# Kernel optimization log

Measured on AMD Instinct MI355X. Metric: run time of the kernel, lower is better.

The kernel has to match this reference:

```python
import jax, jax.numpy as jnp
import numpy as np

N = 50000      # nodes
E = 800000     # edges (before self-loops)
IN_DIM = 128
HID = 64
OUT = 32
HEADS = 8
BN_EPS = 1e-5
NEG_SLOPE = 0.2  # PyG GATConv default


def setup_inputs() -> dict:
    key = jax.random.key(0)
    ks = jax.random.split(key, 24)
    g = lambda k, shape, fan_in: (jax.random.normal(k, shape, jnp.float32) / np.sqrt(fan_in))
    return {
        "x": jax.random.normal(ks[0], (N, IN_DIM), jnp.float32),
        "edge_index": jax.random.randint(ks[1], (2, E), 0, N, dtype=jnp.int64),
        # GCN1
        "gcn1_w": g(ks[2], (IN_DIM, HID), IN_DIM),
        "gcn1_b": jnp.zeros((HID,), jnp.float32),
        # BN1 (eval mode running stats)
        "bn1_gamma": jnp.ones((HID,), jnp.float32),
        "bn1_beta": jnp.zeros((HID,), jnp.float32),
        "bn1_mean": 0.1 * jax.random.normal(ks[3], (HID,), jnp.float32),
        "bn1_var": 0.5 + jax.random.uniform(ks[4], (HID,), jnp.float32),
        # GAT1: heads=8, per-head out=HID, concat=False -> mean over heads
        "gat1_w": g(ks[5], (HID, HEADS * HID), HID),
        "gat1_asrc": g(ks[6], (HEADS, HID), HID),
        "gat1_adst": g(ks[7], (HEADS, HID), HID),
        "gat1_b": jnp.zeros((HID,), jnp.float32),
        # GCN2
        "gcn2_w": g(ks[8], (HID, HID), HID),
        "gcn2_b": jnp.zeros((HID,), jnp.float32),
        # BN2
        "bn2_gamma": jnp.ones((HID,), jnp.float32),
        "bn2_beta": jnp.zeros((HID,), jnp.float32),
        "bn2_mean": 0.1 * jax.random.normal(ks[9], (HID,), jnp.float32),
        "bn2_var": 0.5 + jax.random.uniform(ks[10], (HID,), jnp.float32),
        # GAT2: heads=8, per-head out=OUT, concat=False
        "gat2_w": g(ks[11], (HID, HEADS * OUT), HID),
        "gat2_asrc": g(ks[12], (HEADS, OUT), OUT),
        "gat2_adst": g(ks[13], (HEADS, OUT), OUT),
        "gat2_b": jnp.zeros((OUT,), jnp.float32),
    }


def _gcn(x, src, dst, w, b, n):
    # PyG GCNConv: x @ W, symmetric norm with self-loops (src/dst already include them)
    h = x @ w
    deg = jax.ops.segment_sum(jnp.ones(src.shape[0], x.dtype), dst, num_segments=n)
    dinv = jnp.where(deg > 0, jax.lax.rsqrt(jnp.maximum(deg, 1.0)), 0.0)
    coef = dinv[src] * dinv[dst]                     # [E']
    out = jax.ops.segment_sum(coef[:, None] * h[src], dst, num_segments=n)
    return out + b


def _gat(x, src, dst, w, a_src, a_dst, b, n, heads, ch):
    # PyG GATConv (concat=False): mean over heads, softmax over incoming edges per dst
    h = (x @ w).reshape(n, heads, ch)                # [N,H,C]
    es = jnp.einsum('nhc,hc->nh', h, a_src)          # alpha_src per node
    ed = jnp.einsum('nhc,hc->nh', h, a_dst)
    e = jax.nn.leaky_relu(es[src] + ed[dst], NEG_SLOPE)  # [E',H]
    m = jax.ops.segment_max(e, dst, num_segments=n)
    m = jnp.where(jnp.isfinite(m), m, 0.0)
    ex = jnp.exp(e - m[dst])
    denom = jax.ops.segment_sum(ex, dst, num_segments=n)
    alpha = ex / (denom[dst] + 1e-16)                # [E',H]
    out = jnp.zeros((n, ch), x.dtype)
    for hd in range(heads):  # fixed small head loop keeps peak edge memory at [E',C]
        msg = alpha[:, hd, None] * h[src, hd]        # [E',C]
        out = out + jax.ops.segment_sum(msg, dst, num_segments=n)
    return out / heads + b


def _bn_eval(x, gamma, beta, mean, var):
    return (x - mean) * jax.lax.rsqrt(var + BN_EPS) * gamma + beta


def reference(x, edge_index,
              gcn1_w, gcn1_b, bn1_gamma, bn1_beta, bn1_mean, bn1_var,
              gat1_w, gat1_asrc, gat1_adst, gat1_b,
              gcn2_w, gcn2_b, bn2_gamma, bn2_beta, bn2_mean, bn2_var,
              gat2_w, gat2_asrc, gat2_adst, gat2_b):
    n = x.shape[0]
    loops = jnp.arange(n, dtype=edge_index.dtype)
    src = jnp.concatenate([edge_index[0], loops])    # self-loops (PyG default)
    dst = jnp.concatenate([edge_index[1], loops])

    h = _gcn(x, src, dst, gcn1_w, gcn1_b, n)
    h = jax.nn.relu(_bn_eval(h, bn1_gamma, bn1_beta, bn1_mean, bn1_var))
    h = jax.nn.relu(_gat(h, src, dst, gat1_w, gat1_asrc, gat1_adst, gat1_b, n, HEADS, HID))
    h = _gcn(h, src, dst, gcn2_w, gcn2_b, n)
    h = jax.nn.relu(_bn_eval(h, bn2_gamma, bn2_beta, bn2_mean, bn2_var))
    h = _gat(h, src, dst, gat2_w, gat2_asrc, gat2_adst, gat2_b, n, HEADS, OUT)
    return jax.nn.log_softmax(h, axis=1)
```

## Files before the change

### kernel.cpp

```cpp
#include <hip/hip_runtime.h>
#include <hip/hip_bf16.h>

#define NN 50000
#define NE 800000
#define IND 128
#define NH 8
#define EBLK 256
#define EPB 3125
#define NBUK 391
#define NBUKP 392
#define GH (NBUKP * EBLK)
#define PREPB 308

typedef __hip_bfloat16 bf16;
typedef __attribute__((ext_vector_type(8))) short short8;
typedef __attribute__((ext_vector_type(8))) __bf16 bf16x8;
typedef __attribute__((ext_vector_type(4))) float floatx4;
typedef __attribute__((ext_vector_type(2))) float floatx2;

static __device__ __forceinline__ short f2bf_bits(float f) {
    unsigned u = __float_as_uint(f);
    u = (u + 0x7fffu + ((u >> 16) & 1u)) >> 16;
    return (short)u;
}
// ... 19 lines not shown
static __device__ __forceinline__ void scan_buckets(const int* __restrict__ bsum,
        int* sp, int* gb, int tid) {
    int v0 = (2 * tid < NBUKP) ? bsum[2 * tid] : 0;
    int v1 = (2 * tid + 1 < NBUKP) ? bsum[2 * tid + 1] : 0;
    int c = v0 + v1;
    sp[tid] = c; __syncthreads();
    int val = c;
#pragma unroll
    for (int off = 1; off < 256; off <<= 1) {
        int t = (tid >= off) ? sp[tid - off] : 0;
        __syncthreads();
        val += t; sp[tid] = val;
        __syncthreads();
    }
    int pex = val - c;
    gb[2 * tid] = pex;
    gb[2 * tid + 1] = pex + v0;
    __syncthreads();
}

__global__ __launch_bounds__(256) void bin_count_prep_kernel(const int* __restrict__ edst,
        int* __restrict__ ghist,
        const float* __restrict__ gcn1_w, const float* __restrict__ gcn2_w,
        const float* __restrict__ gat1_w, const float* __restrict__ gat2_w,
        const float* __restrict__ as1, const float* __restrict__ ad1,
        const float* __restrict__ as2, const float* __restrict__ ad2,
        bf16* __restrict__ wT1, bf16* __restrict__ wT2,
        bf16* __restrict__ wgT1, bf16* __restrict__ wgT2,
        float* __restrict__ was1, float* __restrict__ wad1,
        float* __restrict__ was2, float* __restrict__ wad2) {
    __shared__ int hsh[NBUKP];
    const int tid = threadIdx.x;
    if (blockIdx.x < EBLK) {
        const int blk = blockIdx.x;
        for (int b = tid; b < NBUKP; b += 256) hsh[b] = 0;
        __syncthreads();
        const int e0 = blk * EPB;
        for (int e = e0 + tid; e < e0 + EPB; e += 256)
            atomicAdd(&hsh[edst[e] >> 7], 1);
        __syncthreads();
        for (int b = tid; b < NBUKP; b += 256)
            ghist[b * EBLK + blk] = hsh[b];
    } else {
        int idx = (blockIdx.x - EBLK) * 256 + tid;
        if (idx < 8192) {
            int m = idx >> 7, k = idx & 127;
            ((short*)wT1)[idx] = f2bf_bits(gcn1_w[(long)k * 64 + m]);
        } else if (idx < 12288) {
            int i = idx - 8192;
            int m = i >> 6, k = i & 63;
            ((short*)wT2)[i] = f2bf_bits(gcn2_w[(long)k * 64 + m]);
        } else if (idx < 45056) {
            int i = idx - 12288;
            int m = i >> 9, k = i & 511;
            int h = k >> 6, c = k & 63;
            ((short*)wgT1)[i] = f2bf_bits(gat1_w[(long)c * 512 + h * 64 + m]);
        } else if (idx < 77824) {
            int i = idx - 45056;
            int m = i >> 9, k = i & 511;
            int h = k >> 6, c = k & 63;
            ((short*)wgT2)[i] = (m < 32) ? f2bf_bits(gat2_w[(long)c * 256 + h * 32 + m]) : (short)0;
        } else if (idx < 78336) {
            int i = idx - 77824;
            int h = i >> 6, c = i & 63;
            const float* wrow = gat1_w + (long)c * 512 + h * 64;
            float s = 0.f, d = 0.f;
            for (int cc = 0; cc < 64; ++cc) {
                float w = wrow[cc];
                s += w * as1[h * 64 + cc];
                d += w * ad1[h * 64 + cc];
            }
            was1[i] = s; wad1[i] = d;
        } else if (idx < 78848) {
            int i = idx - 78336;
            int h = i >> 6, c = i & 63;
            const float* wrow = gat2_w + (long)c * 256 + h * 32;
            float s = 0.f, d = 0.f;
            for (int cc = 0; cc < 32; ++cc) {
                float w = wrow[cc];
                s += w * as2[h * 32 + cc];
                d += w * ad2[h * 32 + cc];
            }
            was2[i] = s; wad2[i] = d;
        }
    }
}

__global__ __launch_bounds__(256) void scang1_kernel(const int* __restrict__ src,
        int* __restrict__ pre, int* __restrict__ bsum, int n) {
    __shared__ int sh[256];
    const int tid = threadIdx.x;
    const int idx = blockIdx.x * 256 + tid;
    int c = (idx < n) ? src[idx] : 0;
    sh[tid] = c; __syncthreads();
    int val = c;
#pragma unroll
    for (int off = 1; off < 256; off <<= 1) {
        int t = (tid >= off) ? sh[tid - off] : 0;
        __syncthreads();
        val += t; sh[tid] = val;
        __syncthreads();
    }
    if (idx < n) pre[idx] = val - c;
    if (tid == 255) bsum[blockIdx.x] = val;
}

__global__ __launch_bounds__(256) void bin_scatter_kernel(const int* __restrict__ esrc,
        const int* __restrict__ edst, const int* __restrict__ gpre,
        const int* __restrict__ bsum, unsigned* __restrict__ ebuf) {
    __shared__ int cur[NBUKP];
    __shared__ int sp[256], gb[512];
    const int tid = threadIdx.x, blk = blockIdx.x;
    scan_buckets(bsum, sp, gb, tid);
    for (int b = tid; b < NBUKP; b += 256)
        cur[b] = gpre[b * EBLK + blk] + gb[b];
    __syncthreads();
    const int e0 = blk * EPB;
    for (int e = e0 + tid; e < e0 + EPB; e += 256) {
        int d = edst[e], s = esrc[e];
        int pos = atomicAdd(&cur[d >> 7], 1);
        ebuf[pos] = ((unsigned)(d & 127) << 16) | (unsigned)s;
    }
}

__global__ __launch_bounds__(256) void bucket_finalize_kernel(const unsigned* __restrict__ ebuf,
        const int* __restrict__ gpre, const int* __restrict__ bsum,
        int* __restrict__ rowptr, float* __restrict__ dinv, int* __restrict__ csrc) {
    __shared__ int lh[128], lcur[128], sc[256];
    __shared__ int sp[256], gb[512];
    const int bu = blockIdx.x, tid = threadIdx.x;
    scan_buckets(bsum, sp, gb, tid);
    const int seg_beg = gpre[bu * EBLK] + gb[bu];
    const int seg_end = gpre[(bu + 1) * EBLK] + gb[bu + 1];
    if (tid < 128) lh[tid] = 0;
    __syncthreads();
    for (int i = seg_beg + tid; i < seg_end; i += 256)
        atomicAdd(&lh[ebuf[i] >> 16], 1);
    __syncthreads();
    int c = (tid < 128) ? lh[tid] : 0;
    sc[tid] = c; __syncthreads();
    int val = c;
#pragma unroll
    for (int off = 1; off < 256; off <<= 1) {
        int t = (tid >= off) ? sc[tid - off] : 0;
        __syncthreads();
        val += t; sc[tid] = val;
        __syncthreads();
    }
    int excl = val - c;
    if (tid < 128) {
        lcur[tid] = excl;
        int node = bu * 128 + tid;
        if (node < NN) {
            rowptr[node] = seg_beg + excl;
            dinv[node] = rsqrtf((float)c + 1.f);
        }
    }
    if (bu == 0 && tid == 0) rowptr[NN] = NE;
    __syncthreads();
    for (int i = seg_beg + tid; i < seg_end; i += 256) {
        unsigned u = ebuf[i];
        int pos = atomicAdd(&lcur[u >> 16], 1);
        csrc[seg_beg + pos] = (int)(u & 0xffffu);
    }
}

template<int K, int EPI, bool AF32>
__global__ __launch_bounds__(256) void mm2_kernel(const void* __restrict__ A,
        const bf16* __restrict__ wT, void* __restrict__ C,
        const float* __restrict__ bias, const float* __restrict__ rowscale,
        int nrows, int M) {
    const int row0 = blockIdx.x * 64;
    const int tid = threadIdx.x;
    const int lane = tid & 63, wave = tid >> 6;
    const int lr = lane & 15, q = lane >> 4;
    const int row = row0 + wave * 16 + lr;
    const bool rok = row < nrows;
    constexpr int NC = 4;
    floatx4 acc[NC] = {};
#pragma unroll 4
    for (int k0 = 0; k0 < K; k0 += 32) {
        short8 av = {0, 0, 0, 0, 0, 0, 0, 0};
        if (rok) {
            if (AF32) {
                const float* apf = (const float*)A + (long)row * K + q * 8 + k0;
                floatx4 va = *(const floatx4*)apf;
                floatx4 vb = *(const floatx4*)(apf + 4);
#pragma unroll
                for (int j = 0; j < 4; ++j) { av[j] = f2bf_bits(va[j]); av[4 + j] = f2bf_bits(vb[j]); }
            } else {
                av = *(const short8*)((const short*)A + (long)row * K + q * 8 + k0);
            }
        }
        bf16x8 a = __builtin_bit_cast(bf16x8, av);
#pragma unroll
        for (int c = 0; c < NC; ++c) {
            bf16x8 b = __builtin_bit_cast(bf16x8,
                *(const short8*)((const short*)wT + (long)(c * 16 + lr) * K + k0 + q * 8));
            acc[c] = __builtin_amdgcn_mfma_f32_16x16x32_bf16(a, b, acc[c], 0, 0, 0);
        }
    }
#pragma unroll
    for (int c = 0; c < NC; ++c)
#pragma unroll
        for (int r = 0; r < 4; ++r) {
            int orow = row0 + wave * 16 + q * 4 + r;
            int col = c * 16 + lr;
            if (orow < nrows && col < M) {
                long o = (long)orow * M + col;
                float v = acc[c][r];
                if (EPI == 0) ((float*)C)[o] = v;
                else if (EPI == 2) {
                    v = v * 0.125f + bias[col];
                    ((bf16*)C)[o] = __float2bfloat16(fmaxf(v, 0.f));
                } else {
                    ((bf16*)C)[o] = __float2bfloat16(rowscale[orow] * v);
                }
            }
        }
}

__global__ __launch_bounds__(256) void gcn_fused_kernel(const int* __restrict__ rowptr,
        const int* __restrict__ csrc, const float* __restrict__ dinv,
        const bf16* __restrict__ hin, const float* __restrict__ b,
        const float* __restrict__ gamma, const float* __restrict__ beta,
        const float* __restrict__ mean, const float* __restrict__ var,
        bf16* __restrict__ actout) {
    const int node = blockIdx.x * 4 + (threadIdx.x >> 6);
    if (node >= NN) return;
    const int lane = threadIdx.x & 63;
    const int eslot = lane >> 5, cp = lane & 31;
    const unsigned cpo = 4u * (unsigned)cp;
    const int beg = __builtin_amdgcn_readfirstlane(rowptr[node]);
    const int end = __builtin_amdgcn_readfirstlane(rowptr[node + 1]);
    const float di = dinv[node];
    const int* csp = csrc + beg;
    floatx2 acc2 = {0.f, 0.f};
    const int dn = end - beg;
    const int kup = (dn + 15) & ~15;
    for (int k0 = 0; k0 < kup; k0 += 16) {
        int s_[8]; float w_[8];
#pragma unroll
        for (int u = 0; u < 8; ++u) {
            int k = k0 + 2 * u + eslot;
            int ok = k < dn;
            s_[u] = csp[ok ? k : 0];
            w_[u] = ok ? 1.f : 0.f;
        }
        unsigned av_[8];
#pragma unroll
        for (int u = 0; u < 8; ++u)
            av_[u] = *(const unsigned*)((const char*)hin + ((unsigned)s_[u] * 128u + cpo));
#pragma unroll
        for (int u = 0; u < 8; ++u) {
            floatx2 a2 = up2(av_[u]);
            acc2 += a2 * w_[u];
        }
    }
    acc2.x += __shfl_xor(acc2.x, 32);
    acc2.y += __shfl_xor(acc2.y, 32);
    {
        unsigned sv = *(const unsigned*)((const char*)hin + ((unsigned)node * 128u + cpo));
        acc2 += up2(sv);
    }
    int c0 = 2 * cp, c1 = c0 + 1;
    float x0 = acc2.x * di + b[c0];
    float x1 = acc2.y * di + b[c1];
    x0 = (x0 - mean[c0]) * rsqrtf(var[c0] + 1e-5f) * gamma[c0] + beta[c0];
    x1 = (x1 - mean[c1]) * rsqrtf(var[c1] + 1e-5f) * gamma[c1] + beta[c1];
    if (eslot == 0)
        *(unsigned*)((unsigned short*)actout + (long)node * 64 + c0) =
            pk2(fmaxf(x0, 0.f), fmaxf(x1, 0.f));
}

__global__ __launch_bounds__(256) void scores_kernel(const bf16* __restrict__ actb,
        const float* __restrict__ was, const float* __restrict__ wad,
        float* __restrict__ es, float* __restrict__ ed, int n) {
    const int node = blockIdx.x * 4 + (threadIdx.x >> 6);
    if (node >= n) return;
    const int lane = threadIdx.x & 63;
    const int h = lane >> 3, cg = lane & 7;
    short8 a8 = *(const short8*)((const short*)actb + (long)node * 64 + cg * 8);
    const float* wsp = was + h * 64 + cg * 8;
    const float* wdp = wad + h * 64 + cg * 8;
    floatx4 ws0 = *(const floatx4*)wsp, ws1 = *(const floatx4*)(wsp + 4);
    floatx4 wd0 = *(const floatx4*)wdp, wd1 = *(const floatx4*)(wdp + 4);
    float s = 0.f, d = 0.f;
#pragma unroll
    for (int j = 0; j < 4; ++j) {
        float v0 = bf2f(__builtin_bit_cast(bf16, a8[j]));
        float v1 = bf2f(__builtin_bit_cast(bf16, a8[4 + j]));
        s += v0 * ws0[j] + v1 * ws1[j];
        d += v0 * wd0[j] + v1 * wd1[j];
    }
#pragma unroll
    for (int off = 1; off < 8; off <<= 1) {
        s += __shfl_xor(s, off);
        d += __shfl_xor(d, off);
    }
    if (cg == 0) { es[node * NH + h] = s; ed[node * NH + h] = d; }
}

template<int NCT, int EPI>
__global__ __launch_bounds__(256) void gat_fused_kernel(const int* __restrict__ rowptr,
        const int* __restrict__ csrc, const float* __restrict__ es, const float* __restrict__ ed,
        const bf16* __restrict__ actb, const bf16* __restrict__ wgT,
        const float* __restrict__ bias, void* __restrict__ outp) {
    __shared__ __align__(16) float salpha[4][512];
    __shared__ int ssrcs[4][64];
    __shared__ __align__(16) float sself[4][8];
    __shared__ __align__(16) unsigned short aggt[16][520];
    __shared__ float redbuf[2][2][16];
    const int wv = threadIdx.x >> 6;
    const int lane = threadIdx.x & 63;
    const int h = lane & 7, slot = lane >> 3;
    const int hq = lane >> 5, cp = lane & 31;
    const unsigned cpo = 4u * (unsigned)cp;

#pragma unroll 1
    for (int nn = 0; nn < 4; ++nn) {
        const int row = wv * 4 + nn;
        const int node = blockIdx.x * 16 + row;
        const int beg = __builtin_amdgcn_readfirstlane(rowptr[node]);
        const int end = __builtin_amdgcn_readfirstlane(rowptr[node + 1]);
        const int deg = end - beg;
        const int* csp = csrc + beg;
        const float edr = *(const float*)((const char*)ed + ((unsigned)node * 32u + (unsigned)h * 4u));
        float selfe = *(const float*)((const char*)es + ((unsigned)node * 32u + (unsigned)h * 4u)) + edr;
        selfe = selfe > 0.f ? selfe : 0.2f * selfe;

        if (deg <= 64) {
            const int nb = (deg + 7) >> 3;
            const int dm1 = (deg > 0) ? deg - 1 : 0;
            float ex_r[8]; int s_r[8];
            float den = 0.f;
#pragma unroll
            for (int b = 0; b < 8; ++b) { ex_r[b] = 0.f; s_r[b] = 0; }
            if (deg > 0) {
#pragma unroll
                for (int b = 0; b < 8; ++b)
                    if (b < nb) {
                        int k = b * 8 + slot;
                        s_r[b] = csp[k < deg ? k : dm1];
                    }
#pragma unroll
                for (int b = 0; b < 8; ++b)
                    if (b < nb) {
                        float e = *(const float*)((const char*)es +
                                  ((unsigned)s_r[b] * 32u + (unsigned)h * 4u)) + edr;
                        e = e > 0.f ? e : 0.2f * e;
                        float ex = __expf(e - selfe);
                        ex_r[b] = (b * 8 + slot < deg) ? ex : 0.f;
                        den += ex_r[b];
                    }
            }
            den += __shfl_xor(den, 8);
            den += __shfl_xor(den, 16);
            den += __shfl_xor(den, 32);
            const float invden = 1.f / (den + 1.f);
#pragma unroll
            for (int b = 0; b < 8; ++b)
                if (b < nb) salpha[wv][b * 64 + lane] = ex_r[b] * invden;
            if (h == 0) {
#pragma unroll
                for (int b = 0; b < 8; ++b)
                    if (b < nb) ssrcs[wv][b * 8 + slot] = s_r[b];
            }
            if (slot == 0) sself[wv][h] = invden;

            floatx2 acc2[4] = {};
            const int ng = nb;
            if (ng > 0) {
                int sA0, sA1, sA2, sA3, sA4, sA5, sA6, sA7;
                int sB0, sB1, sB2, sB3, sB4, sB5, sB6, sB7;
                unsigned rA0, rA1, rA2, rA3, rA4, rA5, rA6, rA7;
                unsigned rB0, rB1, rB2, rB3, rB4, rB5, rB6, rB7;
#define LOAD_BANK(S, R, G) do { \
    const int* sp_ = &ssrcs[wv][(G) * 8]; \
    S##0 = __builtin_amdgcn_readfirstlane(sp_[0]); \
    S##1 = __builtin_amdgcn_readfirstlane(sp_[1]); \
    S##2 = __builtin_amdgcn_readfirstlane(sp_[2]); \
    S##3 = __builtin_amdgcn_readfirstlane(sp_[3]); \
    S##4 = __builtin_amdgcn_readfirstlane(sp_[4]); \
    S##5 = __builtin_amdgcn_readfirstlane(sp_[5]); \
    S##6 = __builtin_amdgcn_readfirstlane(sp_[6]); \
    S##7 = __builtin_amdgcn_readfirstlane(sp_[7]); \
    R##0 = *(const unsigned*)((const char*)actb + ((unsigned)S##0 * 128u + cpo)); \
    R##1 = *(const unsigned*)((const char*)actb + ((unsigned)S##1 * 128u + cpo)); \
    R##2 = *(const unsigned*)((const char*)actb + ((unsigned)S##2 * 128u + cpo)); \
    R##3 = *(const unsigned*)((const char*)actb + ((unsigned)S##3 * 128u + cpo)); \
    R##4 = *(const unsigned*)((const char*)actb + ((unsigned)S##4 * 128u + cpo)); \
    R##5 = *(const unsigned*)((const char*)actb + ((unsigned)S##5 * 128u + cpo)); \
    R##6 = *(const unsigned*)((const char*)actb + ((unsigned)S##6 * 128u + cpo)); \
    R##7 = *(const unsigned*)((const char*)actb + ((unsigned)S##7 * 128u + cpo)); \
} while (0)
#define FMA_BANK(R, G) do { \
    const float* ab_ = &salpha[wv][(G) * 64 + hq * 4]; \
    unsigned rr_[8] = {R##0, R##1, R##2, R##3, R##4, R##5, R##6, R##7}; \
    _Pragma("unroll") \
    for (int j_ = 0; j_ < 8; ++j_) { \
        floatx4 al_ = *(const floatx4*)(ab_ + j_ * 8); \
        floatx2 al01_ = __builtin_shufflevector(al_, al_, 0, 1); \
        floatx2 al23_ = __builtin_shufflevector(al_, al_, 2, 3); \
        floatx2 a2_ = up2(rr_[j_]); \
        pk_fma_lo(acc2[0], a2_, al01_); pk_fma_hi(acc2[1], a2_, al01_); \
        pk_fma_lo(acc2[2], a2_, al23_); pk_fma_hi(acc2[3], a2_, al23_); \
    } \
} while (0)
                LOAD_BANK(sA, rA, 0);
                int g = 0;
                while (true) {
                    if (g + 1 < ng) LOAD_BANK(sB, rB, g + 1);
                    __builtin_amdgcn_sched_barrier(0);
                    FMA_BANK(rA, g);
                    ++g; if (g >= ng) break;
                    if (g + 1 < ng) LOAD_BANK(sA, rA, g + 1);
                    __builtin_amdgcn_sched_barrier(0);
                    FMA_BANK(rB, g);
                    ++g; if (g >= ng) break;
                }
#undef LOAD_BANK
#undef FMA_BANK
            }
            {
                unsigned sv = *(const unsigned*)((const char*)actb + ((unsigned)node * 128u + cpo));
                floatx2 a2 = up2(sv);
                floatx4 sa = *(const floatx4*)&sself[wv][hq * 4];
                floatx2 sa01 = __builtin_shufflevector(sa, sa, 0, 1);
                floatx2 sa23 = __builtin_shufflevector(sa, sa, 2, 3);
                pk_fma_lo(acc2[0], a2, sa01); pk_fma_hi(acc2[1], a2, sa01);
                pk_fma_lo(acc2[2], a2, sa23); pk_fma_hi(acc2[3], a2, sa23);
            }
#pragma unroll
            for (int j = 0; j < 4; ++j)
                *(unsigned*)&aggt[row][(hq * 4 + j) * 64 + 2 * cp] = pk2(acc2[j].x, acc2[j].y);
        } else {
            float acc[NH] = {0.f, 0.f, 0.f, 0.f, 0.f, 0.f, 0.f, 0.f};
            float den = 0.f;
            for (int base = beg; base < end; base += 8) {
                int ei = base + slot;
                if (ei < end) {
                    int s = csrc[ei];
                    float e = es[s * NH + h] + edr;
                    e = e > 0.f ? e : 0.2f * e;
                    den += __expf(e - selfe);
                }
            }
            den += __shfl_xor(den, 8);
            den += __shfl_xor(den, 16);
            den += __shfl_xor(den, 32);
            const float invden = 1.f / (den + 1.f);
            for (int base = beg; base < end; base += 8) {
                int ei = base + slot;
                float al = 0.f; int sl = 0;
                if (ei < end) {
                    sl = csrc[ei];
                    float e = es[sl * NH + h] + edr;
                    e = e > 0.f ? e : 0.2f * e;
                    al = __expf(e - selfe) * invden;
                }
                salpha[wv][lane] = al;
                if (h == 0) ssrcs[wv][slot] = sl;
                int ecnt = end - base; if (ecnt > 8) ecnt = 8;
                for (int j = 0; j < ecnt; ++j) {
                    int s = ssrcs[wv][j];
                    float a = bf2f(actb[(long)s * 64 + lane]);
                    floatx4 al0 = *(const floatx4*)&salpha[wv][j * 8];
                    floatx4 al1 = *(const floatx4*)&salpha[wv][j * 8 + 4];
                    acc[0] += al0[0] * a; acc[1] += al0[1] * a;
                    acc[2] += al0[2] * a; acc[3] += al0[3] * a;
                    acc[4] += al1[0] * a; acc[5] += al1[1] * a;
                    acc[6] += al1[2] * a; acc[7] += al1[3] * a;
                }
            }
            {
                if (slot == 0) sself[wv][h] = invden;
                float a = bf2f(actb[(long)node * 64 + lane]);
                floatx4 s0 = *(const floatx4*)&sself[wv][0];
                floatx4 s1 = *(const floatx4*)&sself[wv][4];
                acc[0] += s0[0] * a; acc[1] += s0[1] * a;
                acc[2] += s0[2] * a; acc[3] += s0[3] * a;
                acc[4] += s1[0] * a; acc[5] += s1[1] * a;
                acc[6] += s1[2] * a; acc[7] += s1[3] * a;
            }
#pragma unroll
            for (int hh = 0; hh < NH; ++hh)
                aggt[row][hh * 64 + lane] = (unsigned short)f2bf_bits(acc[hh]);
        }
    }

    __syncthreads();

    const int lr = lane & 15, q = lane >> 4;
    const bool act = wv < NCT;
    floatx4 acc = {};
    if (act) {
#pragma unroll 4
        for (int k0 = 0; k0 < 512; k0 += 32) {
            bf16x8 a = __builtin_bit_cast(bf16x8,
                *(const short8*)&aggt[lr][k0 + q * 8]);
            bf16x8 b = __builtin_bit_cast(bf16x8,
                *(const short8*)((const short*)wgT + (long)(wv * 16 + lr) * 512 + k0 + q * 8));
            acc = __builtin_amdgcn_mfma_f32_16x16x32_bf16(a, b, acc, 0, 0, 0);
        }
    }

    if (EPI == 2) {
        if (act) {
#pragma unroll
            for (int r = 0; r < 4; ++r) {
                int node = blockIdx.x * 16 + q * 4 + r;
                int col = wv * 16 + lr;
                float v = acc[r] * 0.125f + bias[col];
                ((bf16*)outp)[(long)node * 64 + col] = __float2bfloat16(fmaxf(v, 0.f));
            }
        }
    } else {
        float v[4], m[4];
#pragma unroll
        for (int r = 0; r < 4; ++r) {
            v[r] = acc[r] * 0.125f + (act ? bias[wv * 16 + lr] : 0.f);
            m[r] = v[r];
        }
#pragma unroll
        for (int off = 1; off < 16; off <<= 1)
#pragma unroll
            for (int r = 0; r < 4; ++r) m[r] = fmaxf(m[r], __shfl_xor(m[r], off));
        if (act && lr == 0) {
#pragma unroll
            for (int r = 0; r < 4; ++r) redbuf[0][wv][q * 4 + r] = m[r];
        }
        __syncthreads();
        float s[4];
#pragma unroll
        for (int r = 0; r < 4; ++r) {
            float mm_ = fmaxf(redbuf[0][0][q * 4 + r], redbuf[0][1][q * 4 + r]);
            m[r] = mm_;
            s[r] = act ? __expf(v[r] - mm_) : 0.f;
        }
#pragma unroll
        for (int off = 1; off < 16; off <<= 1)
#pragma unroll
            for (int r = 0; r < 4; ++r) s[r] += __shfl_xor(s[r], off);
        if (act && lr == 0) {
#pragma unroll
            for (int r = 0; r < 4; ++r) redbuf[1][wv][q * 4 + r] = s[r];
        }
        __syncthreads();
        if (act) {
#pragma unroll
            for (int r = 0; r < 4; ++r) {
                int row = q * 4 + r;
                int node = blockIdx.x * 16 + row;
                float ls = m[r] + logf(redbuf[1][0][row] + redbuf[1][1][row]);
                ((float*)outp)[(long)node * 32 + wv * 16 + lr] = v[r] - ls;
            }
        }
    }
}

extern "C" void kernel_launch(void* const* d_in, const int* in_sizes, int n_in,
                              void* d_out, int out_size, void* d_ws, size_t ws_size,
                              hipStream_t stream) {
    const float* x        = (const float*)d_in[0];
    const int*   eidx     = (const int*)d_in[1];
    const float* gcn1_w   = (const float*)d_in[2];
    const float* gcn1_b   = (const float*)d_in[3];
    const float* bn1_g    = (const float*)d_in[4];
    const float* bn1_b    = (const float*)d_in[5];
    const float* bn1_m    = (const float*)d_in[6];
    const float* bn1_v    = (const float*)d_in[7];
    const float* gat1_w   = (const float*)d_in[8];
    const float* gat1_as  = (const float*)d_in[9];
    const float* gat1_ad  = (const float*)d_in[10];
    const float* gat1_b   = (const float*)d_in[11];
    const float* gcn2_w   = (const float*)d_in[12];
    const float* gcn2_b   = (const float*)d_in[13];
    const float* bn2_g    = (const float*)d_in[14];
    const float* bn2_b    = (const float*)d_in[15];
    const float* bn2_m    = (const float*)d_in[16];
    const float* bn2_v    = (const float*)d_in[17];
    const float* gat2_w   = (const float*)d_in[18];
    const float* gat2_as  = (const float*)d_in[19];
    const float* gat2_ad  = (const float*)d_in[20];
    const float* gat2_b   = (const float*)d_in[21];
    float* out = (float*)d_out;

    const int* esrc = eidx;
    const int* edst = eidx + NE;

    float* ws = (float*)d_ws;
    int*      ghist  = (int*)ws;
    int*      gpre   = ghist + GH;
    int*      gbsum  = gpre + GH;
    unsigned* ebuf   = (unsigned*)(gbsum + 512);
    int*      rowptr = (int*)(ebuf + NE);
    int*      csrc   = rowptr + 50048;
    float*    dinv   = (float*)(csrc + NE);
    float*    es     = dinv + 50048;
    float*    ed     = es + 400000;
    float*    was1   = ed + 400000;
    float*    wad1   = was1 + 512;
    float*    was2   = wad1 + 512;
    float*    wad2   = was2 + 512;
    bf16*     wT1    = (bf16*)(wad2 + 512);
    bf16*     wT2    = wT1 + 64 * 128;
    bf16*     wgT1   = wT2 + 64 * 64;
    bf16*     wgT2   = wgT1 + 64 * 512;
    bf16*     actb   = wgT2 + 64 * 512;
    bf16*     mmbf   = actb + (size_t)NN * 64;
    bf16*     gact   = mmbf + (size_t)NN * 64;

    auto cdiv = [](long a, long b) { return (int)((a + b - 1) / b); };
    const int GB = cdiv(NN, 64);
    const int NB = cdiv(NN, 4);
    const int FB = NN / 16;

    bin_count_prep_kernel<<<EBLK + PREPB, 256, 0, stream>>>(edst, ghist,
        gcn1_w, gcn2_w, gat1_w, gat2_w, gat1_as, gat1_ad, gat2_as, gat2_ad,
        wT1, wT2, wgT1, wgT2, was1, wad1, was2, wad2);
    scang1_kernel<<<GH / 256, 256, 0, stream>>>(ghist, gpre, gbsum, GH);
    bin_scatter_kernel<<<EBLK, 256, 0, stream>>>(esrc, edst, gpre, gbsum, ebuf);
    bucket_finalize_kernel<<<NBUK, 256, 0, stream>>>(ebuf, gpre, gbsum, rowptr, dinv, csrc);

    mm2_kernel<IND, 3, true><<<GB, 256, 0, stream>>>(x, wT1, mmbf, nullptr, dinv, NN, 64);
    gcn_fused_kernel<<<NB, 256, 0, stream>>>(rowptr, csrc, dinv, mmbf,
        gcn1_b, bn1_g, bn1_b, bn1_m, bn1_v, actb);

    scores_kernel<<<NB, 256, 0, stream>>>(actb, was1, wad1, es, ed, NN);
    gat_fused_kernel<4, 2><<<FB, 256, 0, stream>>>(rowptr, csrc, es, ed, actb, wgT1, gat1_b, gact);

    mm2_kernel<64, 3, false><<<GB, 256, 0, stream>>>(gact, wT2, mmbf, nullptr, dinv, NN, 64);
    gcn_fused_kernel<<<NB, 256, 0, stream>>>(rowptr, csrc, dinv, mmbf,
        gcn2_b, bn2_g, bn2_b, bn2_m, bn2_v, actb);

    scores_kernel<<<NB, 256, 0, stream>>>(actb, was2, wad2, es, ed, NN);
    gat_fused_kernel<2, 4><<<FB, 256, 0, stream>>>(rowptr, csrc, es, ed, actb, wgT2, gat2_b, out);
}
```

Baseline: 347.6 us.

## Process four nodes per GAT block instead of sixteen to raise block count

The fused GAT kernel now assigns one node per wavefront (4 nodes per block) instead of looping each wave over 4 nodes (16 per block), quadrupling the grid size. Unused rows of the 16-row aggregation tile are zeroed so the MFMA projection epilogue still runs on a full tile, but only the first 4 rows are written out. The aim is more parallelism and latency hiding for the irregular gather. In exchange, most of the projection matmul work is wasted on zero rows, and each block pays extra fixed costs (zero-fill, reloading weights).

```diff
diff --git a/kernel.cpp b/kernel.cpp
--- a/kernel.cpp
+++ b/kernel.cpp
@@ -353,71 +353,71 @@
     __shared__ int ssrcs[4][64];
     __shared__ __align__(16) float sself[4][8];
     __shared__ __align__(16) unsigned short aggt[16][520];
-    __shared__ float redbuf[2][2][16];
+    __shared__ float redbuf[2][2][4];
     const int wv = threadIdx.x >> 6;
     const int lane = threadIdx.x & 63;
     const int h = lane & 7, slot = lane >> 3;
     const int hq = lane >> 5, cp = lane & 31;
     const unsigned cpo = 4u * (unsigned)cp;
 
-#pragma unroll 1
-    for (int nn = 0; nn < 4; ++nn) {
-        const int row = wv * 4 + nn;
-        const int node = blockIdx.x * 16 + row;
-        const int beg = __builtin_amdgcn_readfirstlane(rowptr[node]);
-        const int end = __builtin_amdgcn_readfirstlane(rowptr[node + 1]);
-        const int deg = end - beg;
-        const int* csp = csrc + beg;
-        const float edr = *(const float*)((const char*)ed + ((unsigned)node * 32u + (unsigned)h * 4u));
-        float selfe = *(const float*)((const char*)es + ((unsigned)node * 32u + (unsigned)h * 4u)) + edr;
-        selfe = selfe > 0.f ? selfe : 0.2f * selfe;
-
-        if (deg <= 64) {
-            const int nb = (deg + 7) >> 3;
-            const int dm1 = (deg > 0) ? deg - 1 : 0;
-            float ex_r[8]; int s_r[8];
-            float den = 0.f;
-#pragma unroll
-            for (int b = 0; b < 8; ++b) { ex_r[b] = 0.f; s_r[b] = 0; }
-            if (deg > 0) {
-#pragma unroll
-                for (int b = 0; b < 8; ++b)
-                    if (b < nb) {
-                        int k = b * 8 + slot;
-                        s_r[b] = csp[k < deg ? k : dm1];
-                    }
-#pragma unroll
-                for (int b = 0; b < 8; ++b)
-                    if (b < nb) {
-                        float e = *(const float*)((const char*)es +
-                                  ((unsigned)s_r[b] * 32u + (unsigned)h * 4u)) + edr;
-                        e = e > 0.f ? e : 0.2f * e;
-                        float ex = __expf(e - selfe);
-                        ex_r[b] = (b * 8 + slot < deg) ? ex : 0.f;
-                        den += ex_r[b];
-                    }
-            }
-            den += __shfl_xor(den, 8);
-            den += __shfl_xor(den, 16);
-            den += __shfl_xor(den, 32);
-            const float invden = 1.f / (den + 1.f);
+    for (int i = threadIdx.x; i < 12 * 260; i += 256)
+        ((unsigned*)&aggt[4][0])[i] = 0u;
+
+    const int node = blockIdx.x * 4 + wv;
+    const int beg = __builtin_amdgcn_readfirstlane(rowptr[node]);
+    const int end = __builtin_amdgcn_readfirstlane(rowptr[node + 1]);
+    const int deg = end - beg;
+    const int* csp = csrc + beg;
+    const float edr = *(const float*)((const char*)ed + ((unsigned)node * 32u + (unsigned)h * 4u));
+    float selfe = *(const float*)((const char*)es + ((unsigned)node * 32u + (unsigned)h * 4u)) + edr;
+    selfe = selfe > 0.f ? selfe : 0.2f * selfe;
+
+    if (deg <= 64) {
+        const int nb = (deg + 7) >> 3;
+        const int dm1 = (deg > 0) ? deg - 1 : 0;
+        float ex_r[8]; int s_r[8];
+        float den = 0.f;
+#pragma unroll
+        for (int b = 0; b < 8; ++b) { ex_r[b] = 0.f; s_r[b] = 0; }
+        if (deg > 0) {
 #pragma unroll
             for (int b = 0; b < 8; ++b)
-                if (b < nb) salpha[wv][b * 64 + lane] = ex_r[b] * invden;
-            if (h == 0) {
-#pragma unroll
-                for (int b = 0; b < 8; ++b)
-                    if (b < nb) ssrcs[wv][b * 8 + slot] = s_r[b];
-            }
-            if (slot == 0) sself[wv][h] = invden;
-
-            floatx2 acc2[4] = {};
-            const int ng = nb;
-            if (ng > 0) {
-                int sA0, sA1, sA2, sA3, sA4, sA5, sA6, sA7;
-                int sB0, sB1, sB2, sB3, sB4, sB5, sB6, sB7;
-                unsigned rA0, rA1, rA2, rA3, rA4, rA5, rA6, rA7;
-                unsigned rB0, rB1, rB2, rB3, rB4, rB5, rB6, rB7;
+                if (b < nb) {
+                    int k = b * 8 + slot;
+                    s_r[b] = csp[k < deg ? k : dm1];
+                }
+#pragma unroll
+            for (int b = 0; b < 8; ++b)
+                if (b < nb) {
+                    float e = *(const float*)((const char*)es +
+                              ((unsigned)s_r[b] * 32u + (unsigned)h * 4u)) + edr;
+                    e = e > 0.f ? e : 0.2f * e;
+                    float ex = __expf(e - selfe);
+                    ex_r[b] = (b * 8 + slot < deg) ? ex : 0.f;
+                    den += ex_r[b];
+                }
+        }
+        den += __shfl_xor(den, 8);
+        den += __shfl_xor(den, 16);
+        den += __shfl_xor(den, 32);
+        const float invden = 1.f / (den + 1.f);
+#pragma unroll
+        for (int b = 0; b < 8; ++b)
+            if (b < nb) salpha[wv][b * 64 + lane] = ex_r[b] * invden;
+        if (h == 0) {
+#pragma unroll
+            for (int b = 0; b < 8; ++b)
+                if (b < nb) ssrcs[wv][b * 8 + slot] = s_r[b];
+        }
+        if (slot == 0) sself[wv][h] = invden;
+
+        floatx2 acc2[4] = {};
+        const int ng = nb;
+        if (ng > 0) {
+            int sA0, sA1, sA2, sA3, sA4, sA5, sA6, sA7;
+            int sB0, sB1, sB2, sB3, sB4, sB5, sB6, sB7;
+            unsigned rA0, rA1, rA2, rA3, rA4, rA5, rA6, rA7;
+            unsigned rB0, rB1, rB2, rB3, rB4, rB5, rB6, rB7;
 #define LOAD_BANK(S, R, G) do { \
     const int* sp_ = &ssrcs[wv][(G) * 8]; \
     S##0 = __builtin_amdgcn_readfirstlane(sp_[0]); \
@@ -450,86 +450,85 @@
         pk_fma_lo(acc2[2], a2_, al23_); pk_fma_hi(acc2[3], a2_, al23_); \
     } \
 } while (0)
-                LOAD_BANK(sA, rA, 0);
-                int g = 0;
-                while (true) {
-                    if (g + 1 < ng) LOAD_BANK(sB, rB, g + 1);
-                    __builtin_amdgcn_sched_barrier(0);
-                    FMA_BANK(rA, g);
-                    ++g; if (g >= ng) break;
-                    if (g + 1 < ng) LOAD_BANK(sA, rA, g + 1);
-                    __builtin_amdgcn_sched_barrier(0);
-                    FMA_BANK(rB, g);
-                    ++g; if (g >= ng) break;
-                }
+            LOAD_BANK(sA, rA, 0);
+            int g = 0;
+            while (true) {
+                if (g + 1 < ng) LOAD_BANK(sB, rB, g + 1);
+                __builtin_amdgcn_sched_barrier(0);
+                FMA_BANK(rA, g);
+                ++g; if (g >= ng) break;
+                if (g + 1 < ng) LOAD_BANK(sA, rA, g + 1);
+                __builtin_amdgcn_sched_barrier(0);
+                FMA_BANK(rB, g);
+                ++g; if (g >= ng) break;
+            }
 #undef LOAD_BANK
 #undef FMA_BANK
-            }
-            {
-                unsigned sv = *(const unsigned*)((const char*)actb + ((unsigned)node * 128u + cpo));
-                floatx2 a2 = up2(sv);
-                floatx4 sa = *(const floatx4*)&sself[wv][hq * 4];
-                floatx2 sa01 = __builtin_shufflevector(sa, sa, 0, 1);
-                floatx2 sa23 = __builtin_shufflevector(sa, sa, 2, 3);
-                pk_fma_lo(acc2[0], a2, sa01); pk_fma_hi(acc2[1], a2, sa01);
-                pk_fma_lo(acc2[2], a2, sa23); pk_fma_hi(acc2[3], a2, sa23);
-            }
-#pragma unroll
-            for (int j = 0; j < 4; ++j)
-                *(unsigned*)&aggt[row][(hq * 4 + j) * 64 + 2 * cp] = pk2(acc2[j].x, acc2[j].y);
-        } else {
-            float acc[NH] = {0.f, 0.f, 0.f, 0.f, 0.f, 0.f, 0.f, 0.f};
-            float den = 0.f;
-            for (int base = beg; base < end; base += 8) {
-                int ei = base + slot;
-                if (ei < end) {
-                    int s = csrc[ei];
-                    float e = es[s * NH + h] + edr;
-                    e = e > 0.f ? e : 0.2f * e;
-                    den += __expf(e - selfe);
-                }
-            }
-            den += __shfl_xor(den, 8);
-            den += __shfl_xor(den, 16);
-            den += __shfl_xor(den, 32);
-            const float invden = 1.f / (den + 1.f);
-            for (int base = beg; base < end; base += 8) {
-                int ei = base + slot;
-                float al = 0.f; int sl = 0;
-                if (ei < end) {
-                    sl = csrc[ei];
-                    float e = es[sl * NH + h] + edr;
-                    e = e > 0.f ? e : 0.2f * e;
-                    al = __expf(e - selfe) * invden;
-                }
-                salpha[wv][lane] = al;
-                if (h == 0) ssrcs[wv][slot] = sl;
-                int ecnt = end - base; if (ecnt > 8) ecnt = 8;
-                for (int j = 0; j < ecnt; ++j) {
-                    int s = ssrcs[wv][j];
-                    float a = bf2f(actb[(long)s * 64 + lane]);
-                    floatx4 al0 = *(const floatx4*)&salpha[wv][j * 8];
-                    floatx4 al1 = *(const floatx4*)&salpha[wv][j * 8 + 4];
-                    acc[0] += al0[0] * a; acc[1] += al0[1] * a;
-                    acc[2] += al0[2] * a; acc[3] += al0[3] * a;
-                    acc[4] += al1[0] * a; acc[5] += al1[1] * a;
-                    acc[6] += al1[2] * a; acc[7] += al1[3] * a;
-                }
-            }
-            {
-                if (slot == 0) sself[wv][h] = invden;
-                float a = bf2f(actb[(long)node * 64 + lane]);
-                floatx4 s0 = *(const floatx4*)&sself[wv][0];
-                floatx4 s1 = *(const floatx4*)&sself[wv][4];
-                acc[0] += s0[0] * a; acc[1] += s0[1] * a;
-                acc[2] += s0[2] * a; acc[3] += s0[3] * a;
-                acc[4] += s1[0] * a; acc[5] += s1[1] * a;
-                acc[6] += s1[2] * a; acc[7] += s1[3] * a;
-            }
-#pragma unroll
-            for (int hh = 0; hh < NH; ++hh)
-                aggt[row][hh * 64 + lane] = (unsigned short)f2bf_bits(acc[hh]);
-        }
+        }
+        {
+            unsigned sv = *(const unsigned*)((const char*)actb + ((unsigned)node * 128u + cpo));
+            floatx2 a2 = up2(sv);
+            floatx4 sa = *(const floatx4*)&sself[wv][hq * 4];
+            floatx2 sa01 = __builtin_shufflevector(sa, sa, 0, 1);
+            floatx2 sa23 = __builtin_shufflevector(sa, sa, 2, 3);
+            pk_fma_lo(acc2[0], a2, sa01); pk_fma_hi(acc2[1], a2, sa01);
+            pk_fma_lo(acc2[2], a2, sa23); pk_fma_hi(acc2[3], a2, sa23);
+        }
+#pragma unroll
+        for (int j = 0; j < 4; ++j)
+            *(unsigned*)&aggt[wv][(hq * 4 + j) * 64 + 2 * cp] = pk2(acc2[j].x, acc2[j].y);
+    } else {
+        float acc[NH] = {0.f, 0.f, 0.f, 0.f, 0.f, 0.f, 0.f, 0.f};
+        float den = 0.f;
+        for (int base = beg; base < end; base += 8) {
+            int ei = base + slot;
+            if (ei < end) {
+                int s = csrc[ei];
+                float e = es[s * NH + h] + edr;
+                e = e > 0.f ? e : 0.2f * e;
+                den += __expf(e - selfe);
+            }
+        }
+        den += __shfl_xor(den, 8);
+        den += __shfl_xor(den, 16);
+        den += __shfl_xor(den, 32);
+        const float invden = 1.f / (den + 1.f);
+        for (int base = beg; base < end; base += 8) {
+            int ei = base + slot;
+            float al = 0.f; int sl = 0;
+            if (ei < end) {
+                sl = csrc[ei];
+                float e = es[sl * NH + h] + edr;
+                e = e > 0.f ? e : 0.2f * e;
+                al = __expf(e - selfe) * invden;
+            }
+            salpha[wv][lane] = al;
+            if (h == 0) ssrcs[wv][slot] = sl;
+            int ecnt = end - base; if (ecnt > 8) ecnt = 8;
+            for (int j = 0; j < ecnt; ++j) {
+                int s = ssrcs[wv][j];
+                float a = bf2f(actb[(long)s * 64 + lane]);
+                floatx4 al0 = *(const floatx4*)&salpha[wv][j * 8];
+                floatx4 al1 = *(const floatx4*)&salpha[wv][j * 8 + 4];
+                acc[0] += al0[0] * a; acc[1] += al0[1] * a;
+                acc[2] += al0[2] * a; acc[3] += al0[3] * a;
+                acc[4] += al1[0] * a; acc[5] += al1[1] * a;
+                acc[6] += al1[2] * a; acc[7] += al1[3] * a;
+            }
+        }
+        {
+            if (slot == 0) sself[wv][h] = invden;
+            float a = bf2f(actb[(long)node * 64 + lane]);
+            floatx4 s0 = *(const floatx4*)&sself[wv][0];
+            floatx4 s1 = *(const floatx4*)&sself[wv][4];
+            acc[0] += s0[0] * a; acc[1] += s0[1] * a;
+            acc[2] += s0[2] * a; acc[3] += s0[3] * a;
+            acc[4] += s1[0] * a; acc[5] += s1[1] * a;
+            acc[6] += s1[2] * a; acc[7] += s1[3] * a;
+        }
+#pragma unroll
+        for (int hh = 0; hh < NH; ++hh)
+            aggt[wv][hh * 64 + lane] = (unsigned short)f2bf_bits(acc[hh]);
     }
 
     __syncthreads();
@@ -549,13 +548,13 @@
     }
 
     if (EPI == 2) {
-        if (act) {
+        if (act && q == 0) {
 #pragma unroll
             for (int r = 0; r < 4; ++r) {
-                int node = blockIdx.x * 16 + q * 4 + r;
+                int onode = blockIdx.x * 4 + r;
                 int col = wv * 16 + lr;
                 float v = acc[r] * 0.125f + bias[col];
-                ((bf16*)outp)[(long)node * 64 + col] = __float2bfloat16(fmaxf(v, 0.f));
+                ((bf16*)outp)[(long)onode * 64 + col] = __float2bfloat16(fmaxf(v, 0.f));
             }
         }
     } else {
@@ -569,15 +568,15 @@
         for (int off = 1; off < 16; off <<= 1)
 #pragma unroll
             for (int r = 0; r < 4; ++r) m[r] = fmaxf(m[r], __shfl_xor(m[r], off));
-        if (act && lr == 0) {
-#pragma unroll
-            for (int r = 0; r < 4; ++r) redbuf[0][wv][q * 4 + r] = m[r];
+        if (act && q == 0 && lr == 0) {
+#pragma unroll
+            for (int r = 0; r < 4; ++r) redbuf[0][wv][r] = m[r];
         }
         __syncthreads();
         float s[4];
 #pragma unroll
         for (int r = 0; r < 4; ++r) {
-            float mm_ = fmaxf(redbuf[0][0][q * 4 + r], redbuf[0][1][q * 4 + r]);
+            float mm_ = fmaxf(redbuf[0][0][r], redbuf[0][1][r]);
             m[r] = mm_;
             s[r] = act ? __expf(v[r] - mm_) : 0.f;
         }
@@ -585,18 +584,17 @@
         for (int off = 1; off < 16; off <<= 1)
 #pragma unroll
             for (int r = 0; r < 4; ++r) s[r] += __shfl_xor(s[r], off);
-        if (act && lr == 0) {
-#pragma unroll
-            for (int r = 0; r < 4; ++r) redbuf[1][wv][q * 4 + r] = s[r];
-        }
-        __syncthreads();
-        if (act) {
+        if (act && q == 0 && lr == 0) {
+#pragma unroll
+            for (int r = 0; r < 4; ++r) redbuf[1][wv][r] = s[r];
+        }
+        __syncthreads();
+        if (act && q == 0) {
 #pragma unroll
             for (int r = 0; r < 4; ++r) {
-                int row = q * 4 + r;
-                int node = blockIdx.x * 16 + row;
-                float ls = m[r] + logf(redbuf[1][0][row] + redbuf[1][1][row]);
-                ((float*)outp)[(long)node * 32 + wv * 16 + lr] = v[r] - ls;
+                int onode = blockIdx.x * 4 + r;
+                float ls = m[r] + logf(redbuf[1][0][r] + redbuf[1][1][r]);
+                ((float*)outp)[(long)onode * 32 + wv * 16 + lr] = v[r] - ls;
             }
         }
     }
@@ -657,7 +655,7 @@
     auto cdiv = [](long a, long b) { return (int)((a + b - 1) / b); };
     const int GB = cdiv(NN, 64);
     const int NB = cdiv(NN, 4);
-    const int FB = NN / 16;
+    const int FB = NN / 4;
 
     bin_count_prep_kernel<<<EBLK + PREPB, 256, 0, stream>>>(edst, ghist,
         gcn1_w, gcn2_w, gat1_w, gat2_w, gat1_as, gat1_ad, gat2_as, gat2_ad,
```

After: 417.7 us. 20.2% more time.

## Give each GAT node its own wavefront using 1024-thread blocks

Applied to the files above, without the earlier changes.

The fused GAT kernel now launches 1024-thread blocks in which each of the 16 waves handles one node, instead of 4 waves each looping over 4 nodes in turn. Shared-memory staging arrays grow to per-wave size for 16 waves. The aim is to expose more independent gathers at once and hide gather latency through wave-level parallelism rather than a serial per-wave node loop. The readfirstlane scalarisation of source indices and the sched_barrier fences in the double-buffered gather loop are also removed. This trades higher LDS use per block and coarser block scheduling, and it depends on the unseen epilogue correctly ignoring waves beyond the original four.

```diff
diff --git a/kernel.cpp b/kernel.cpp
--- a/kernel.cpp
+++ b/kernel.cpp
@@ -345,13 +345,13 @@
 }
 
 template<int NCT, int EPI>
-__global__ __launch_bounds__(256) void gat_fused_kernel(const int* __restrict__ rowptr,
+__global__ __launch_bounds__(1024) void gat_fused_kernel(const int* __restrict__ rowptr,
         const int* __restrict__ csrc, const float* __restrict__ es, const float* __restrict__ ed,
         const bf16* __restrict__ actb, const bf16* __restrict__ wgT,
         const float* __restrict__ bias, void* __restrict__ outp) {
-    __shared__ __align__(16) float salpha[4][512];
-    __shared__ int ssrcs[4][64];
-    __shared__ __align__(16) float sself[4][8];
+    __shared__ __align__(16) float salpha[16][512];
+    __shared__ int ssrcs[16][64];
+    __shared__ __align__(16) float sself[16][8];
     __shared__ __align__(16) unsigned short aggt[16][520];
     __shared__ float redbuf[2][2][16];
     const int wv = threadIdx.x >> 6;
@@ -360,74 +360,65 @@
     const int hq = lane >> 5, cp = lane & 31;
     const unsigned cpo = 4u * (unsigned)cp;
 
-#pragma unroll 1
-    for (int nn = 0; nn < 4; ++nn) {
-        const int row = wv * 4 + nn;
-        const int node = blockIdx.x * 16 + row;
-        const int beg = __builtin_amdgcn_readfirstlane(rowptr[node]);
-        const int end = __builtin_amdgcn_readfirstlane(rowptr[node + 1]);
-        const int deg = end - beg;
-        const int* csp = csrc + beg;
-        const float edr = *(const float*)((const char*)ed + ((unsigned)node * 32u + (unsigned)h * 4u));
-        float selfe = *(const float*)((const char*)es + ((unsigned)node * 32u + (unsigned)h * 4u)) + edr;
-        selfe = selfe > 0.f ? selfe : 0.2f * selfe;
-
-        if (deg <= 64) {
-            const int nb = (deg + 7) >> 3;
-            const int dm1 = (deg > 0) ? deg - 1 : 0;
-            float ex_r[8]; int s_r[8];
-            float den = 0.f;
-#pragma unroll
-            for (int b = 0; b < 8; ++b) { ex_r[b] = 0.f; s_r[b] = 0; }
-            if (deg > 0) {
-#pragma unroll
-                for (int b = 0; b < 8; ++b)
-                    if (b < nb) {
-                        int k = b * 8 + slot;
-                        s_r[b] = csp[k < deg ? k : dm1];
-                    }
-#pragma unroll
-                for (int b = 0; b < 8; ++b)
-                    if (b < nb) {
-                        float e = *(const float*)((const char*)es +
-                                  ((unsigned)s_r[b] * 32u + (unsigned)h * 4u)) + edr;
-                        e = e > 0.f ? e : 0.2f * e;
-                        float ex = __expf(e - selfe);
-                        ex_r[b] = (b * 8 + slot < deg) ? ex : 0.f;
-                        den += ex_r[b];
-                    }
-            }
-            den += __shfl_xor(den, 8);
-            den += __shfl_xor(den, 16);
-            den += __shfl_xor(den, 32);
-            const float invden = 1.f / (den + 1.f);
+    const int node = blockIdx.x * 16 + wv;
+    const int beg = __builtin_amdgcn_readfirstlane(rowptr[node]);
+    const int end = __builtin_amdgcn_readfirstlane(rowptr[node + 1]);
+    const int deg = end - beg;
+    const int* csp = csrc + beg;
+    const float edr = *(const float*)((const char*)ed + ((unsigned)node * 32u + (unsigned)h * 4u));
+    float selfe = *(const float*)((const char*)es + ((unsigned)node * 32u + (unsigned)h * 4u)) + edr;
+    selfe = selfe > 0.f ? selfe : 0.2f * selfe;
+
+    if (deg <= 64) {
+        const int nb = (deg + 7) >> 3;
+        const int dm1 = (deg > 0) ? deg - 1 : 0;
+        float ex_r[8]; int s_r[8];
+        float den = 0.f;
+#pragma unroll
+        for (int b = 0; b < 8; ++b) { ex_r[b] = 0.f; s_r[b] = 0; }
+        if (deg > 0) {
 #pragma unroll
             for (int b = 0; b < 8; ++b)
-                if (b < nb) salpha[wv][b * 64 + lane] = ex_r[b] * invden;
-            if (h == 0) {
-#pragma unroll
-                for (int b = 0; b < 8; ++b)
-                    if (b < nb) ssrcs[wv][b * 8 + slot] = s_r[b];
-            }
-            if (slot == 0) sself[wv][h] = invden;
-
-            floatx2 acc2[4] = {};
-            const int ng = nb;
-            if (ng > 0) {
-                int sA0, sA1, sA2, sA3, sA4, sA5, sA6, sA7;
-                int sB0, sB1, sB2, sB3, sB4, sB5, sB6, sB7;
-                unsigned rA0, rA1, rA2, rA3, rA4, rA5, rA6, rA7;
-                unsigned rB0, rB1, rB2, rB3, rB4, rB5, rB6, rB7;
+                if (b < nb) {
+                    int k = b * 8 + slot;
+                    s_r[b] = csp[k < deg ? k : dm1];
+                }
+#pragma unroll
+            for (int b = 0; b < 8; ++b)
+                if (b < nb) {
+                    float e = *(const float*)((const char*)es +
+                              ((unsigned)s_r[b] * 32u + (unsigned)h * 4u)) + edr;
+                    e = e > 0.f ? e : 0.2f * e;
+                    float ex = __expf(e - selfe);
+                    ex_r[b] = (b * 8 + slot < deg) ? ex : 0.f;
+                    den += ex_r[b];
+                }
+        }
+        den += __shfl_xor(den, 8);
+        den += __shfl_xor(den, 16);
+        den += __shfl_xor(den, 32);
+        const float invden = 1.f / (den + 1.f);
+#pragma unroll
+        for (int b = 0; b < 8; ++b)
+            if (b < nb) salpha[wv][b * 64 + lane] = ex_r[b] * invden;
+        if (h == 0) {
+#pragma unroll
+            for (int b = 0; b < 8; ++b)
+                if (b < nb) ssrcs[wv][b * 8 + slot] = s_r[b];
+        }
+        if (slot == 0) sself[wv][h] = invden;
+
+        floatx2 acc2[4] = {};
+        const int ng = nb;
+        if (ng > 0) {
+            int sA0, sA1, sA2, sA3, sA4, sA5, sA6, sA7;
+            int sB0, sB1, sB2, sB3, sB4, sB5, sB6, sB7;
+            unsigned rA0, rA1, rA2, rA3, rA4, rA5, rA6, rA7;
+            unsigned rB0, rB1, rB2, rB3, rB4, rB5, rB6, rB7;
 #define LOAD_BANK(S, R, G) do { \
     const int* sp_ = &ssrcs[wv][(G) * 8]; \
-    S##0 = __builtin_amdgcn_readfirstlane(sp_[0]); \
-    S##1 = __builtin_amdgcn_readfirstlane(sp_[1]); \
-    S##2 = __builtin_amdgcn_readfirstlane(sp_[2]); \
-    S##3 = __builtin_amdgcn_readfirstlane(sp_[3]); \
-    S##4 = __builtin_amdgcn_readfirstlane(sp_[4]); \
-    S##5 = __builtin_amdgcn_readfirstlane(sp_[5]); \
-    S##6 = __builtin_amdgcn_readfirstlane(sp_[6]); \
-    S##7 = __builtin_amdgcn_readfirstlane(sp_[7]); \
+    S##0 = sp_[0]; S##1 = sp_[1]; S##2 = sp_[2]; S##3 = sp_[3]; \
+    S##4 = sp_[4]; S##5 = sp_[5]; S##6 = sp_[6]; S##7 = sp_[7]; \
     R##0 = *(const unsigned*)((const char*)actb + ((unsigned)S##0 * 128u + cpo)); \
     R##1 = *(const unsigned*)((const char*)actb + ((unsigned)S##1 * 128u + cpo)); \
     R##2 = *(const unsigned*)((const char*)actb + ((unsigned)S##2 * 128u + cpo)); \
@@ -450,86 +441,83 @@
         pk_fma_lo(acc2[2], a2_, al23_); pk_fma_hi(acc2[3], a2_, al23_); \
     } \
 } while (0)
-                LOAD_BANK(sA, rA, 0);
-                int g = 0;
-                while (true) {
-                    if (g + 1 < ng) LOAD_BANK(sB, rB, g + 1);
-                    __builtin_amdgcn_sched_barrier(0);
-                    FMA_BANK(rA, g);
-                    ++g; if (g >= ng) break;
-                    if (g + 1 < ng) LOAD_BANK(sA, rA, g + 1);
-                    __builtin_amdgcn_sched_barrier(0);
-                    FMA_BANK(rB, g);
-                    ++g; if (g >= ng) break;
-                }
+            LOAD_BANK(sA, rA, 0);
+            int g = 0;
+            while (true) {
+                if (g + 1 < ng) LOAD_BANK(sB, rB, g + 1);
+                FMA_BANK(rA, g);
+                ++g; if (g >= ng) break;
+                if (g + 1 < ng) LOAD_BANK(sA, rA, g + 1);
+                FMA_BANK(rB, g);
+                ++g; if (g >= ng) break;
+            }
 #undef LOAD_BANK
 #undef FMA_BANK
-            }
-            {
-                unsigned sv = *(const unsigned*)((const char*)actb + ((unsigned)node * 128u + cpo));
-                floatx2 a2 = up2(sv);
-                floatx4 sa = *(const floatx4*)&sself[wv][hq * 4];
-                floatx2 sa01 = __builtin_shufflevector(sa, sa, 0, 1);
-                floatx2 sa23 = __builtin_shufflevector(sa, sa, 2, 3);
-                pk_fma_lo(acc2[0], a2, sa01); pk_fma_hi(acc2[1], a2, sa01);
-                pk_fma_lo(acc2[2], a2, sa23); pk_fma_hi(acc2[3], a2, sa23);
-            }
-#pragma unroll
-            for (int j = 0; j < 4; ++j)
-                *(unsigned*)&aggt[row][(hq * 4 + j) * 64 + 2 * cp] = pk2(acc2[j].x, acc2[j].y);
-        } else {
-            float acc[NH] = {0.f, 0.f, 0.f, 0.f, 0.f, 0.f, 0.f, 0.f};
-            float den = 0.f;
-            for (int base = beg; base < end; base += 8) {
-                int ei = base + slot;
-                if (ei < end) {
-                    int s = csrc[ei];
-                    float e = es[s * NH + h] + edr;
-                    e = e > 0.f ? e : 0.2f * e;
-                    den += __expf(e - selfe);
-                }
-            }
-            den += __shfl_xor(den, 8);
-            den += __shfl_xor(den, 16);
-            den += __shfl_xor(den, 32);
-            const float invden = 1.f / (den + 1.f);
-            for (int base = beg; base < end; base += 8) {
-                int ei = base + slot;
-                float al = 0.f; int sl = 0;
-                if (ei < end) {
-                    sl = csrc[ei];
-                    float e = es[sl * NH + h] + edr;
-                    e = e > 0.f ? e : 0.2f * e;
-                    al = __expf(e - selfe) * invden;
-                }
-                salpha[wv][lane] = al;
-                if (h == 0) ssrcs[wv][slot] = sl;
-                int ecnt = end - base; if (ecnt > 8) ecnt = 8;
-                for (int j = 0; j < ecnt; ++j) {
-                    int s = ssrcs[wv][j];
-                    float a = bf2f(actb[(long)s * 64 + lane]);
-                    floatx4 al0 = *(const floatx4*)&salpha[wv][j * 8];
-                    floatx4 al1 = *(const floatx4*)&salpha[wv][j * 8 + 4];
-                    acc[0] += al0[0] * a; acc[1] += al0[1] * a;
-                    acc[2] += al0[2] * a; acc[3] += al0[3] * a;
-                    acc[4] += al1[0] * a; acc[5] += al1[1] * a;
-                    acc[6] += al1[2] * a; acc[7] += al1[3] * a;
-                }
-            }
-            {
-                if (slot == 0) sself[wv][h] = invden;
-                float a = bf2f(actb[(long)node * 64 + lane]);
-                floatx4 s0 = *(const floatx4*)&sself[wv][0];
-                floatx4 s1 = *(const floatx4*)&sself[wv][4];
-                acc[0] += s0[0] * a; acc[1] += s0[1] * a;
-                acc[2] += s0[2] * a; acc[3] += s0[3] * a;
-                acc[4] += s1[0] * a; acc[5] += s1[1] * a;
-                acc[6] += s1[2] * a; acc[7] += s1[3] * a;
-            }
-#pragma unroll
-            for (int hh = 0; hh < NH; ++hh)
-                aggt[row][hh * 64 + lane] = (unsigned short)f2bf_bits(acc[hh]);
-        }
+        }
+        {
+            unsigned sv = *(const unsigned*)((const char*)actb + ((unsigned)node * 128u + cpo));
+            floatx2 a2 = up2(sv);
+            floatx4 sa = *(const floatx4*)&sself[wv][hq * 4];
+            floatx2 sa01 = __builtin_shufflevector(sa, sa, 0, 1);
+            floatx2 sa23 = __builtin_shufflevector(sa, sa, 2, 3);
+            pk_fma_lo(acc2[0], a2, sa01); pk_fma_hi(acc2[1], a2, sa01);
+            pk_fma_lo(acc2[2], a2, sa23); pk_fma_hi(acc2[3], a2, sa23);
+        }
+#pragma unroll
+        for (int j = 0; j < 4; ++j)
+            *(unsigned*)&aggt[wv][(hq * 4 + j) * 64 + 2 * cp] = pk2(acc2[j].x, acc2[j].y);
+    } else {
+        float acc[NH] = {0.f, 0.f, 0.f, 0.f, 0.f, 0.f, 0.f, 0.f};
+        float den = 0.f;
+        for (int base = beg; base < end; base += 8) {
+            int ei = base + slot;
+            if (ei < end) {
+                int s = csrc[ei];
+                float e = es[s * NH + h] + edr;
+                e = e > 0.f ? e : 0.2f * e;
+                den += __expf(e - selfe);
+            }
+        }
+        den += __shfl_xor(den, 8);
+        den += __shfl_xor(den, 16);
+        den += __shfl_xor(den, 32);
+        const float invden = 1.f / (den + 1.f);
+        for (int base = beg; base < end; base += 8) {
+            int ei = base + slot;
+            float al = 0.f; int sl = 0;
+            if (ei < end) {
+                sl = csrc[ei];
+                float e = es[sl * NH + h] + edr;
+                e = e > 0.f ? e : 0.2f * e;
+                al = __expf(e - selfe) * invden;
+            }
+            salpha[wv][lane] = al;
+            if (h == 0) ssrcs[wv][slot] = sl;
+            int ecnt = end - base; if (ecnt > 8) ecnt = 8;
+            for (int j = 0; j < ecnt; ++j) {
+                int s = ssrcs[wv][j];
+                float a = bf2f(actb[(long)s * 64 + lane]);
+                floatx4 al0 = *(const floatx4*)&salpha[wv][j * 8];
+                floatx4 al1 = *(const floatx4*)&salpha[wv][j * 8 + 4];
+                acc[0] += al0[0] * a; acc[1] += al0[1] * a;
+                acc[2] += al0[2] * a; acc[3] += al0[3] * a;
+                acc[4] += al1[0] * a; acc[5] += al1[1] * a;
+                acc[6] += al1[2] * a; acc[7] += al1[3] * a;
+            }
+        }
+        {
+            if (slot == 0) sself[wv][h] = invden;
+            float a = bf2f(actb[(long)node * 64 + lane]);
+            floatx4 s0 = *(const floatx4*)&sself[wv][0];
+            floatx4 s1 = *(const floatx4*)&sself[wv][4];
+            acc[0] += s0[0] * a; acc[1] += s0[1] * a;
+            acc[2] += s0[2] * a; acc[3] += s0[3] * a;
+            acc[4] += s1[0] * a; acc[5] += s1[1] * a;
+            acc[6] += s1[2] * a; acc[7] += s1[3] * a;
+        }
+#pragma unroll
+        for (int hh = 0; hh < NH; ++hh)
+            aggt[wv][hh * 64 + lane] = (unsigned short)f2bf_bits(acc[hh]);
     }
 
     __syncthreads();
@@ -552,10 +540,10 @@
         if (act) {
 #pragma unroll
             for (int r = 0; r < 4; ++r) {
-                int node = blockIdx.x * 16 + q * 4 + r;
+                int onode = blockIdx.x * 16 + q * 4 + r;
                 int col = wv * 16 + lr;
                 float v = acc[r] * 0.125f + bias[col];
-                ((bf16*)outp)[(long)node * 64 + col] = __float2bfloat16(fmaxf(v, 0.f));
+                ((bf16*)outp)[(long)onode * 64 + col] = __float2bfloat16(fmaxf(v, 0.f));
             }
         }
     } else {
@@ -594,9 +582,9 @@
 #pragma unroll
             for (int r = 0; r < 4; ++r) {
                 int row = q * 4 + r;
-                int node = blockIdx.x * 16 + row;
+                int onode = blockIdx.x * 16 + row;
                 float ls = m[r] + logf(redbuf[1][0][row] + redbuf[1][1][row]);
-                ((float*)outp)[(long)node * 32 + wv * 16 + lr] = v[r] - ls;
+                ((float*)outp)[(long)onode * 32 + wv * 16 + lr] = v[r] - ls;
             }
         }
     }
@@ -671,12 +659,12 @@
         gcn1_b, bn1_g, bn1_b, bn1_m, bn1_v, actb);
 
     scores_kernel<<<NB, 256, 0, stream>>>(actb, was1, wad1, es, ed, NN);
-    gat_fused_kernel<4, 2><<<FB, 256, 0, stream>>>(rowptr, csrc, es, ed, actb, wgT1, gat1_b, gact);
+    gat_fused_kernel<4, 2><<<FB, 1024, 0, stream>>>(rowptr, csrc, es, ed, actb, wgT1, gat1_b, gact);
 
     mm2_kernel<64, 3, false><<<GB, 256, 0, stream>>>(gact, wT2, mmbf, nullptr, dinv, NN, 64);
     gcn_fused_kernel<<<NB, 256, 0, stream>>>(rowptr, csrc, dinv, mmbf,
         gcn2_b, bn2_g, bn2_b, bn2_m, bn2_v, actb);
 
     scores_kernel<<<NB, 256, 0, stream>>>(actb, was2, wad2, es, ed, NN);
-    gat_fused_kernel<2, 4><<<FB, 256, 0, stream>>>(rowptr, csrc, es, ed, actb, wgT2, gat2_b, out);
-}
+    gat_fused_kernel<2, 4><<<FB, 1024, 0, stream>>>(rowptr, csrc, es, ed, actb, wgT2, gat2_b, out);
+}
```

After: 348.8 us. About the same (+0.3%).
